# Optimization experiments

Measured on AMD Instinct MI355X. Metric: run time of the kernel, lower is better.

The kernel has to match this reference:

```python
import jax, jax.numpy as jnp
import numpy as np

# dims
B, W, L = 64, 64, 16          # sentences, words per sentence, max chars per word
E, H, V = 128, 512, 256       # char_embedding_size, word_embedding_size, char vocab


def setup_inputs() -> dict:
    key = jax.random.key(0)
    ks = jax.random.split(key, 8)
    chars = jax.random.randint(ks[0], (B, W, L), 1, V)          # char ids (0 = pad, unused in valid region)
    word_lens = jax.random.randint(ks[1], (B, W), 1, L + 1)     # per-word char counts in [1, L]
    emb = (jax.random.normal(ks[2], (V, E), jnp.float32) * 0.1).at[0].set(0.0)  # padding_idx=0 -> zero row

    def lstm_params(k):
        k1, k2, k3, k4 = jax.random.split(k, 4)
        s = 1.0 / np.sqrt(H)
        return (jax.random.uniform(k1, (4 * H, E), jnp.float32, -s, s),
                jax.random.uniform(k2, (4 * H, H), jnp.float32, -s, s),
                jax.random.uniform(k3, (4 * H,), jnp.float32, -s, s),
                jax.random.uniform(k4, (4 * H,), jnp.float32, -s, s))

    Wih_f, Whh_f, bih_f, bhh_f = lstm_params(ks[3])
    Wih_b, Whh_b, bih_b, bhh_b = lstm_params(ks[4])
    s = 1.0 / np.sqrt(2 * H)
    Wp = jax.random.uniform(ks[5], (H, 2 * H), jnp.float32, -s, s)
    bp = jax.random.uniform(ks[6], (H,), jnp.float32, -s, s)
    return dict(chars=chars, word_lens=word_lens, emb=emb,
                Wih_f=Wih_f, Whh_f=Whh_f, bih_f=bih_f, bhh_f=bhh_f,
                Wih_b=Wih_b, Whh_b=Whh_b, bih_b=bih_b, bhh_b=bhh_b,
                Wp=Wp, bp=bp)


def _lstm_last(x, lens, Wih, Whh, b):
    """Run a batched LSTM over x [N,L,E]; return hidden state at step lens-1 -> [N,H].
    PyTorch gate order: i, f, g, o."""
    N = x.shape[0]
    xw = jnp.einsum('nle,ge->nlg', x, Wih) + b  # [N, L, 4H], input projections precomputed

    def step(carry, xt):
        h, c = carry
        g = xt + h @ Whh.T
        i, f, gg, o = jnp.split(g, 4, axis=-1)
        c = jax.nn.sigmoid(f) * c + jax.nn.sigmoid(i) * jnp.tanh(gg)
        h = jax.nn.sigmoid(o) * jnp.tanh(c)
        return (h, c), h

    init = (jnp.zeros((N, H), x.dtype), jnp.zeros((N, H), x.dtype))
    _, hs = jax.lax.scan(step, init, jnp.swapaxes(xw, 0, 1))  # [L, N, H]
    hs = jnp.swapaxes(hs, 0, 1)                               # [N, L, H]
    idx = jnp.broadcast_to((lens - 1)[:, None, None], (N, 1, H))
    return jnp.take_along_axis(hs, idx, axis=1)[:, 0]


def reference(chars, word_lens, emb, Wih_f, Whh_f, bih_f, bhh_f,
              Wih_b, Whh_b, bih_b, bhh_b, Wp, bp):
    N = B * W
    lens = word_lens.reshape(N)
    x = emb[chars.reshape(N, L)]  # [N, L, E] char embeddings (dropout is identity in eval)

    # forward direction: hidden at last valid char (padded steps come after, don't matter)
    h_fwd = _lstm_last(x, lens, Wih_f, Whh_f, bih_f + bhh_f)

    # backward direction == forward LSTM over the length-aware reversed word,
    # taking hidden at step lens-1 (matches pack_sequence backward output at pos 0)
    t = jnp.arange(L)
    rev_idx = jnp.clip(lens[:, None] - 1 - t[None, :], 0, L - 1)  # [N, L]
    x_rev = jnp.take_along_axis(x, rev_idx[:, :, None], axis=1)
    h_bwd = _lstm_last(x_rev, lens, Wih_b, Whh_b, bih_b + bhh_b)

    concat = jnp.concatenate([h_bwd, h_fwd], axis=-1)  # torch order: (reverse, forward)
    out = concat @ Wp.T + bp                            # [N, H]
    return out.reshape(B, W, H)
```

## Files before the change

kernel.cpp:

```cpp
#include <hip/hip_runtime.h>

typedef unsigned short u16;
typedef __bf16 bf16x8 __attribute__((ext_vector_type(8)));
typedef float f32x4 __attribute__((ext_vector_type(4)));

#define NW 4096
#define HDIM 512
#define EDIM 128
#define G4 2048
#define LMAX 16
#define KREC 640

__device__ __forceinline__ u16 f2bf(float f) {
  unsigned u = __float_as_uint(f);
  u += 0x7FFFu + ((u >> 16) & 1u);
  return (u16)(u >> 16);
}

__device__ __forceinline__ float sigf(float x) { return 1.f / (1.f + __expf(-x)); }
__device__ __forceinline__ float tanha(float x) {
  float ax = fabsf(x);
  float e = __expf(2.f * ax);
  float t = 1.f - 2.f / (e + 1.f);
  return x < 0.f ? -t : t;
}

__device__ __forceinline__ void gload16(const void* g, void* l) {
  __builtin_amdgcn_global_load_lds((const __attribute__((address_space(1))) void*)g,
                                   (__attribute__((address_space(3))) void*)l, 16, 0, 0);
}

union V16 { int4 i; bf16x8 b; };
__device__ __forceinline__ bf16x8 ldfrag(const u16* p) {
  V16 v; v.i = *(const int4*)p; return v.b;
}

__global__ __launch_bounds__(256) void prep_kernel(
    const int* __restrict__ chars, const int* __restrict__ lens,
    const float* __restrict__ emb,
    const float* __restrict__ Wih_f, const float* __restrict__ Whh_f,
    const float* __restrict__ bih_f, const float* __restrict__ bhh_f,
    const float* __restrict__ Wih_b, const float* __restrict__ Whh_b,
    const float* __restrict__ bih_b, const float* __restrict__ bhh_b,
    const float* __restrict__ Wp,
    u16* __restrict__ Wcat, float* __restrict__ bcat, u16* __restrict__ Wpb,
    u16* __restrict__ Xf, u16* __restrict__ Xb) {
  int idx = blockIdx.x * 256 + threadIdx.x;
  if (idx < 327680) {
    int d = idx / (2048 * 80);
    int r = idx % (2048 * 80);
    int p = r / 80, c8 = r % 80;
    int unit = p >> 2, gate = p & 3;
    int orig = gate * 512 + unit;
    const float* Wih = d ? Wih_b : Wih_f;
    const float* Whh = d ? Whh_b : Whh_f;
    int k = c8 * 8;
    const float* src = (k < EDIM) ? (Wih + (size_t)orig * EDIM + k)
                                  : (Whh + (size_t)orig * HDIM + (k - EDIM));
    union { u16 u[8]; int4 v; } t;
#pragma unroll
    for (int j = 0; j < 8; ++j) t.u[j] = f2bf(src[j]);
    *(int4*)(Wcat + ((size_t)d * G4 + p) * KREC + k) = t.v;
  } else if (idx < 331776) {
    int r = idx - 327680;
    int d = r / G4, p = r % G4;
    int unit = p >> 2, gate = p & 3;
    int orig = gate * 512 + unit;
    bcat[d * G4 + p] = d ? (bih_b[orig] + bhh_b[orig]) : (bih_f[orig] + bhh_f[orig]);
  } else if (idx < 397312) {
    int r = idx - 331776;
    int row = r >> 7, c8 = r & 127;
    union { u16 u[8]; int4 v; } t;
#pragma unroll
    for (int j = 0; j < 8; ++j) t.u[j] = f2bf(Wp[(size_t)row * 1024 + c8 * 8 + j]);
    *(int4*)(Wpb + (size_t)row * 1024 + c8 * 8) = t.v;
  } else {
    int r = idx - 397312;
    int tw = r >> 4, e8 = (r & 15) * 8;
    int t = tw >> 12, w = tw & (NW - 1);
    int len = lens[w];
    int cf = chars[w * LMAX + t];
    int tb = len - 1 - t; if (tb < 0) tb = 0;
    int cb = chars[w * LMAX + tb];
    union { u16 u[8]; int4 v; } vf, vb;
#pragma unroll
    for (int j = 0; j < 8; ++j) {
      vf.u[j] = f2bf(emb[(size_t)cf * EDIM + e8 + j]);
      vb.u[j] = f2bf(emb[(size_t)cb * EDIM + e8 + j]);
    }
    size_t o = ((size_t)t * NW + w) * EDIM + e8;
    *(int4*)(Xf + o) = vf.v;
    *(int4*)(Xb + o) = vb.v;
  }
}

__global__ __launch_bounds__(256) void step_kernel(
    const u16* __restrict__ Wcat, const float* __restrict__ bcat,
    const u16* __restrict__ Xf, const u16* __restrict__ Xb,
    const u16* __restrict__ hprev, u16* __restrict__ hnext,
    float* __restrict__ cst, u16* __restrict__ concat,
    const int* __restrict__ lens, int t, int nIter, int first) {
  __shared__ u16 ldsA[128 * 64];
  __shared__ u16 ldsB[128 * 64];

  const int tid = threadIdx.x;
  const int lane = tid & 63;
  const int wid = tid >> 6;
  const int wm = wid >> 1, wn = wid & 1;
  const int dir = blockIdx.z;
  const int m0 = blockIdx.y * 128;
  const int w0 = blockIdx.x * 128;

  const u16* Wd = Wcat + (size_t)dir * G4 * KREC;
  const u16* Xd = dir ? Xb : Xf;
  const u16* hpd = hprev + (size_t)dir * NW * HDIM;

  f32x4 acc[4][4];
#pragma unroll
  for (int i = 0; i < 4; ++i)
#pragma unroll
    for (int j = 0; j < 4; ++j) acc[i][j] = (f32x4){0.f, 0.f, 0.f, 0.f};

  const int srow = tid >> 3;
  const int c8 = tid & 7;

  for (int kit = 0; kit < nIter; ++kit) {
    const int k0 = kit * 64;
#pragma unroll
    for (int s = 0; s < 4; ++s) {
      int rr = s * 32 + srow;
      gload16(Wd + (size_t)(m0 + rr) * KREC + k0 + c8 * 8, ldsA + rr * 64 + c8 * 8);
    }
#pragma unroll
    for (int s = 0; s < 4; ++s) {
      int rr = s * 32 + srow;
      int word = w0 + rr;
      int k = k0 + c8 * 8;
      const u16* src = (k < EDIM) ? (Xd + ((size_t)t * NW + word) * EDIM + k)
                                  : (hpd + (size_t)word * HDIM + (k - EDIM));
      gload16(src, ldsB + rr * 64 + c8 * 8);
    }
    __syncthreads();
#pragma unroll
    for (int kk = 0; kk < 2; ++kk) {
      const int ko = kk * 32 + (lane >> 4) * 8;
      bf16x8 af[4], bfr[4];
#pragma unroll
      for (int mi = 0; mi < 4; ++mi)
        af[mi] = ldfrag(ldsA + (wm * 64 + mi * 16 + (lane & 15)) * 64 + ko);
#pragma unroll
      for (int ni = 0; ni < 4; ++ni)
        bfr[ni] = ldfrag(ldsB + (wn * 64 + ni * 16 + (lane & 15)) * 64 + ko);
#pragma unroll
      for (int mi = 0; mi < 4; ++mi)
#pragma unroll
        for (int ni = 0; ni < 4; ++ni)
          acc[mi][ni] = __builtin_amdgcn_mfma_f32_16x16x32_bf16(af[mi], bfr[ni], acc[mi][ni], 0, 0, 0);
    }
    __syncthreads();
  }

  const float* bcd = bcat + dir * G4;
  float* cd = cst + (size_t)dir * HDIM * NW;
  u16* hstage = ldsA;
#pragma unroll
  for (int mi = 0; mi < 4; ++mi) {
    int ul = wm * 16 + mi * 4 + (lane >> 4);
    int unit = blockIdx.y * 32 + ul;
    float4 bb = *(const float4*)(bcd + 4 * unit);
#pragma unroll
    for (int ni = 0; ni < 4; ++ni) {
      int wl = wn * 64 + ni * 16 + (lane & 15);
      int word = w0 + wl;
      f32x4 a = acc[mi][ni];
      float gi = a[0] + bb.x, gf = a[1] + bb.y, gg = a[2] + bb.z, go = a[3] + bb.w;
      size_t cidx = (size_t)unit * NW + word;
      float c0 = first ? 0.f : cd[cidx];
      float cn = sigf(gf) * c0 + sigf(gi) * tanha(gg);
      float hh = sigf(go) * tanha(cn);
      cd[cidx] = cn;
      hstage[wl * 32 + ul] = f2bf(hh);
    }
  }
  __syncthreads();

  u16* hnd = hnext + (size_t)dir * NW * HDIM;
  const int dirOff = dir ? 0 : HDIM;
#pragma unroll
  for (int r = 0; r < 2; ++r) {
    int i4 = tid * 2 + r;
    int wl = i4 >> 2, part = i4 & 3;
    int word = w0 + wl;
    int4 v = ((const int4*)hstage)[i4];
    *(int4*)(hnd + (size_t)word * HDIM + blockIdx.y * 32 + part * 8) = v;
    if (t == lens[word] - 1)
      *(int4*)(concat + (size_t)word * 1024 + dirOff + blockIdx.y * 32 + part * 8) = v;
  }
}

__global__ __launch_bounds__(256) void proj_kernel(
    const u16* __restrict__ concat, const u16* __restrict__ Wpb,
    const float* __restrict__ bp, float* __restrict__ out) {
  __shared__ u16 ldsA[128 * 64];
  __shared__ u16 ldsB[128 * 64];

  const int tid = threadIdx.x;
  const int lane = tid & 63;
  const int wid = tid >> 6;
  const int wm = wid >> 1, wn = wid & 1;
  const int m0 = blockIdx.x * 128;
  const int n0 = blockIdx.y * 128;

  f32x4 acc[4][4];
#pragma unroll
  for (int i = 0; i < 4; ++i)
#pragma unroll
    for (int j = 0; j < 4; ++j) acc[i][j] = (f32x4){0.f, 0.f, 0.f, 0.f};

  const int srow = tid >> 3;
  const int c8 = tid & 7;

  for (int kit = 0; kit < 16; ++kit) {
    const int k0 = kit * 64;
#pragma unroll
    for (int s = 0; s < 4; ++s) {
      int rr = s * 32 + srow;
      gload16(concat + (size_t)(m0 + rr) * 1024 + k0 + c8 * 8, ldsA + rr * 64 + c8 * 8);
      gload16(Wpb + (size_t)(n0 + rr) * 1024 + k0 + c8 * 8, ldsB + rr * 64 + c8 * 8);
    }
    __syncthreads();
#pragma unroll
    for (int kk = 0; kk < 2; ++kk) {
      const int ko = kk * 32 + (lane >> 4) * 8;
      bf16x8 af[4], bfr[4];
#pragma unroll
      for (int mi = 0; mi < 4; ++mi)
        af[mi] = ldfrag(ldsA + (wm * 64 + mi * 16 + (lane & 15)) * 64 + ko);
#pragma unroll
      for (int ni = 0; ni < 4; ++ni)
        bfr[ni] = ldfrag(ldsB + (wn * 64 + ni * 16 + (lane & 15)) * 64 + ko);
#pragma unroll
      for (int mi = 0; mi < 4; ++mi)
#pragma unroll
        for (int ni = 0; ni < 4; ++ni)
          acc[mi][ni] = __builtin_amdgcn_mfma_f32_16x16x32_bf16(af[mi], bfr[ni], acc[mi][ni], 0, 0, 0);
    }
    __syncthreads();
  }

  float bpv[4];
#pragma unroll
  for (int ni = 0; ni < 4; ++ni) bpv[ni] = bp[n0 + wn * 64 + ni * 16 + (lane & 15)];
#pragma unroll
  for (int mi = 0; mi < 4; ++mi)
#pragma unroll
    for (int ni = 0; ni < 4; ++ni)
#pragma unroll
      for (int rg = 0; rg < 4; ++rg) {
        int word = m0 + wm * 64 + mi * 16 + (lane >> 4) * 4 + rg;
        int hout = n0 + wn * 64 + ni * 16 + (lane & 15);
        out[(size_t)word * HDIM + hout] = acc[mi][ni][rg] + bpv[ni];
      }
}

extern "C" void kernel_launch(void* const* d_in, const int* in_sizes, int n_in,
                              void* d_out, int out_size, void* d_ws, size_t ws_size,
                              hipStream_t stream) {
  const int* chars = (const int*)d_in[0];
  const int* lens  = (const int*)d_in[1];
  const float* emb = (const float*)d_in[2];
  const float* Wih_f = (const float*)d_in[3];
  const float* Whh_f = (const float*)d_in[4];
  const float* bih_f = (const float*)d_in[5];
  const float* bhh_f = (const float*)d_in[6];
  const float* Wih_b = (const float*)d_in[7];
  const float* Whh_b = (const float*)d_in[8];
  const float* bih_b = (const float*)d_in[9];
  const float* bhh_b = (const float*)d_in[10];
  const float* Wp = (const float*)d_in[11];
  const float* bp = (const float*)d_in[12];
  float* out = (float*)d_out;

  char* ws = (char*)d_ws;
  size_t o = 0;
  u16* Wcat = (u16*)(ws + o);  o += (size_t)2 * G4 * KREC * 2;
  float* bcat = (float*)(ws + o); o += (size_t)2 * G4 * 4;
  u16* Wpb = (u16*)(ws + o);   o += (size_t)HDIM * 1024 * 2;
  u16* Xf = (u16*)(ws + o);    o += (size_t)LMAX * NW * EDIM * 2;
  u16* Xb = (u16*)(ws + o);    o += (size_t)LMAX * NW * EDIM * 2;
  u16* hbuf = (u16*)(ws + o);  o += (size_t)2 * 2 * NW * HDIM * 2;
  float* cst = (float*)(ws + o); o += (size_t)2 * HDIM * NW * 4;
  u16* concat = (u16*)(ws + o); o += (size_t)NW * 1024 * 2;

  prep_kernel<<<5648, 256, 0, stream>>>(chars, lens, emb,
      Wih_f, Whh_f, bih_f, bhh_f, Wih_b, Whh_b, bih_b, bhh_b, Wp,
      Wcat, bcat, Wpb, Xf, Xb);

  const size_t hping = (size_t)2 * NW * HDIM;
  for (int t = 0; t < LMAX; ++t) {
    int ping = t & 1;
    u16* hprev = hbuf + (size_t)ping * hping;
    u16* hnext = hbuf + (size_t)(ping ^ 1) * hping;
    int nIter = (t == 0) ? 2 : 10;
    step_kernel<<<dim3(32, 16, 2), 256, 0, stream>>>(
        Wcat, bcat, Xf, Xb, hprev, hnext, cst, concat, lens, t, nIter, t == 0 ? 1 : 0);
  }

  proj_kernel<<<dim3(32, 4), 256, 0, stream>>>(concat, Wpb, bp, out);
}
```

Measured before the change: 844.3 us.

## Sort words by length and skip finished tiles in LSTM steps

```diff
diff --git a/kernel.cpp b/kernel.cpp
--- a/kernel.cpp
+++ b/kernel.cpp
@@ -35,8 +35,37 @@
   V16 v; v.i = *(const int4*)p; return v.b;
 }
 
+__global__ __launch_bounds__(256) void sort_kernel(
+    const int* __restrict__ lens,
+    int* __restrict__ perm, int* __restrict__ lens_s, int* __restrict__ nactive) {
+  __shared__ int cnt[LMAX + 1];
+  __shared__ int start[LMAX + 1];
+  __shared__ int cursor[LMAX + 1];
+  int tid = threadIdx.x;
+  if (tid <= LMAX) cnt[tid] = 0;
+  __syncthreads();
+  for (int w = tid; w < NW; w += 256) atomicAdd(&cnt[lens[w]], 1);
+  __syncthreads();
+  if (tid == 0) {
+    int acc = 0;
+    for (int l = LMAX; l >= 1; --l) { start[l] = acc; acc += cnt[l]; }
+    start[0] = acc;
+  }
+  __syncthreads();
+  if (tid <= LMAX) cursor[tid] = start[tid];
+  if (tid < LMAX) nactive[tid] = start[tid];
+  __syncthreads();
+  for (int w = tid; w < NW; w += 256) {
+    int l = lens[w];
+    int pos = atomicAdd(&cursor[l], 1);
+    perm[pos] = w;
+    lens_s[pos] = l;
+  }
+}
+
 __global__ __launch_bounds__(256) void prep_kernel(
-    const int* __restrict__ chars, const int* __restrict__ lens,
+    const int* __restrict__ chars,
+    const int* __restrict__ perm, const int* __restrict__ lens_s,
     const float* __restrict__ emb,
     const float* __restrict__ Wih_f, const float* __restrict__ Whh_f,
     const float* __restrict__ bih_f, const float* __restrict__ bhh_f,
@@ -77,8 +106,9 @@
   } else {
     int r = idx - 397312;
     int tw = r >> 4, e8 = (r & 15) * 8;
-    int t = tw >> 12, w = tw & (NW - 1);
-    int len = lens[w];
+    int t = tw >> 12, s = tw & (NW - 1);
+    int w = perm[s];
+    int len = lens_s[s];
     int cf = chars[w * LMAX + t];
     int tb = len - 1 - t; if (tb < 0) tb = 0;
     int cb = chars[w * LMAX + tb];
@@ -88,7 +118,7 @@
       vf.u[j] = f2bf(emb[(size_t)cf * EDIM + e8 + j]);
       vb.u[j] = f2bf(emb[(size_t)cb * EDIM + e8 + j]);
     }
-    size_t o = ((size_t)t * NW + w) * EDIM + e8;
+    size_t o = ((size_t)t * NW + s) * EDIM + e8;
     *(int4*)(Xf + o) = vf.v;
     *(int4*)(Xb + o) = vb.v;
   }
@@ -99,7 +129,11 @@
     const u16* __restrict__ Xf, const u16* __restrict__ Xb,
     const u16* __restrict__ hprev, u16* __restrict__ hnext,
     float* __restrict__ cst, u16* __restrict__ concat,
-    const int* __restrict__ lens, int t, int nIter, int first) {
+    const int* __restrict__ perm, const int* __restrict__ lens_s,
+    const int* __restrict__ nactive, int t, int nIter, int first) {
+  const int w0 = blockIdx.x * 128;
+  if (w0 >= nactive[t]) return;
+
   __shared__ u16 ldsA[128 * 64];
   __shared__ u16 ldsB[128 * 64];
 
@@ -109,7 +143,6 @@
   const int wm = wid >> 1, wn = wid & 1;
   const int dir = blockIdx.z;
   const int m0 = blockIdx.y * 128;
-  const int w0 = blockIdx.x * 128;
 
   const u16* Wd = Wcat + (size_t)dir * G4 * KREC;
   const u16* Xd = dir ? Xb : Xf;
@@ -193,8 +226,10 @@
     int word = w0 + wl;
     int4 v = ((const int4*)hstage)[i4];
     *(int4*)(hnd + (size_t)word * HDIM + blockIdx.y * 32 + part * 8) = v;
-    if (t == lens[word] - 1)
-      *(int4*)(concat + (size_t)word * 1024 + dirOff + blockIdx.y * 32 + part * 8) = v;
+    if (t == lens_s[word] - 1) {
+      int orig = perm[word];
+      *(int4*)(concat + (size_t)orig * 1024 + dirOff + blockIdx.y * 32 + part * 8) = v;
+    }
   }
 }
 
@@ -291,8 +326,13 @@
   u16* hbuf = (u16*)(ws + o);  o += (size_t)2 * 2 * NW * HDIM * 2;
   float* cst = (float*)(ws + o); o += (size_t)2 * HDIM * NW * 4;
   u16* concat = (u16*)(ws + o); o += (size_t)NW * 1024 * 2;
-
-  prep_kernel<<<5648, 256, 0, stream>>>(chars, lens, emb,
+  int* perm = (int*)(ws + o);  o += (size_t)NW * 4;
+  int* lens_s = (int*)(ws + o); o += (size_t)NW * 4;
+  int* nactive = (int*)(ws + o); o += 64;
+
+  sort_kernel<<<1, 256, 0, stream>>>(lens, perm, lens_s, nactive);
+
+  prep_kernel<<<5648, 256, 0, stream>>>(chars, perm, lens_s, emb,
       Wih_f, Whh_f, bih_f, bhh_f, Wih_b, Whh_b, bih_b, bhh_b, Wp,
       Wcat, bcat, Wpb, Xf, Xb);
 
@@ -303,7 +343,8 @@
     u16* hnext = hbuf + (size_t)(ping ^ 1) * hping;
     int nIter = (t == 0) ? 2 : 10;
     step_kernel<<<dim3(32, 16, 2), 256, 0, stream>>>(
-        Wcat, bcat, Xf, Xb, hprev, hnext, cst, concat, lens, t, nIter, t == 0 ? 1 : 0);
+        Wcat, bcat, Xf, Xb, hprev, hnext, cst, concat,
+        perm, lens_s, nactive, t, nIter, t == 0 ? 1 : 0);
   }
 
   proj_kernel<<<dim3(32, 4), 256, 0, stream>>>(concat, Wpb, bp, out);
```

New measurement: 851.3 us. No clear change (+0.8%).
